# Performance work log

Measured on AMD Instinct MI355X. Metric: run time of the kernel, lower is better.

## Reference

```python
import jax, jax.numpy as jnp
import numpy as np

NA = 50000
NB = 50000
E = 800000
D = 256


def setup_inputs() -> dict:
    key = jax.random.key(0)
    ks = jax.random.split(key, 7)
    feature_a = jax.random.normal(ks[0], (NA, D), dtype=jnp.float32)
    feature_b = jax.random.normal(ks[1], (NB, D), dtype=jnp.float32)
    # Linear(b_dim, b_dim): store weight pre-transposed so new_emb = feature_b @ W + b
    W = jax.random.normal(ks[2], (D, D), dtype=jnp.float32) * (1.0 / np.sqrt(D))
    b = jnp.zeros((D,), dtype=jnp.float32)
    # kaiming-normal-ish init for attention vector a: [a_dim + b_dim, 1]
    a = jax.random.normal(ks[3], (2 * D, 1), dtype=jnp.float32) * np.sqrt(2.0 / (2 * D))
    edge_src = jnp.sort(jax.random.randint(ks[4], (E,), 0, NA, dtype=jnp.int32)).astype(jnp.int64)
    edge_dst = jax.random.randint(ks[5], (E,), 0, NB, dtype=jnp.int64)
    return {
        "feature_a": feature_a,
        "feature_b": feature_b,
        "W": W,
        "b": b,
        "a": a,
        "edge_src": edge_src,
        "edge_dst": edge_dst,
        "node_num_a": NA,
        "node_num_b": NB,
    }


def reference(feature_a, feature_b, W, b, a, edge_src, edge_dst, node_num_a, node_num_b):
    # new_emb = out_mlp_layer(feature_b)
    new_emb = feature_b @ W + b  # [Nb, D]

    # cat([feature_a[src], new_emb[dst]]) @ a  ==  (feature_a @ a_top)[src] + (new_emb @ a_bot)[dst]
    a_dim = feature_a.shape[1]
    a_top = a[:a_dim, 0]   # [a_dim]
    a_bot = a[a_dim:, 0]   # [b_dim]
    s_a = feature_a @ a_top   # [Na]
    s_b = new_emb @ a_bot     # [Nb]
    logits = s_a[edge_src] + s_b[edge_dst]  # [E]

    # exp(elu(x, alpha=0.1))
    elu = jnp.where(logits > 0, logits, 0.1 * jnp.expm1(logits))
    score = jnp.exp(elu)  # [E]

    # sparse mm: weighted aggregation of new_emb over edges, grouped by src
    msg = score[:, None] * new_emb[edge_dst]  # [E, D]
    agg = jax.ops.segment_sum(msg, edge_src, num_segments=node_num_a)       # [Na, D]
    row_sum = jax.ops.segment_sum(score, edge_src, num_segments=node_num_a)  # [Na]
    row_sum = jnp.where(row_sum == 0, 1.0, row_sum)[:, None]
    return agg / row_sum
```

## Files before the change

### kernel.cpp

```cpp
#include <hip/hip_runtime.h>
#include <cstdint>

#define NA_N 50000
#define NB_N 50000
#define NE_N 800000
#define DD 256
#define GEMM_NBLK 782
#define WT_NBLK   32
#define RS_NBLK   3125
#define SA_NBLK   3125

using bf8   = __attribute__((ext_vector_type(8))) short;
using f32x4 = __attribute__((ext_vector_type(4))) float;
using u16x8 = __attribute__((ext_vector_type(8))) ushort;

__device__ __forceinline__ ushort f2bf(float f) {
    uint u = __float_as_uint(f);
    uint r = (u + 0x7fffu + ((u >> 16) & 1u)) >> 16;
    return (ushort)r;
}
__device__ __forceinline__ float bf2f(ushort u) {
    return __uint_as_float(((uint)u) << 16);
}

__global__ __launch_bounds__(256) void prep_k(const float* __restrict__ W,
    ushort* __restrict__ Wt, const int* __restrict__ esrc,
    int* __restrict__ row_start, const float* __restrict__ fa,
    const float* __restrict__ a_top, float* __restrict__ s_a)
{
    const int t = threadIdx.x;
    if (blockIdx.x < WT_NBLK) {
        const int k0 = blockIdx.x * 8;
        u16x8 pack;
#pragma unroll
        for (int j = 0; j < 8; j++)
            pack[j] = f2bf(W[(size_t)(k0 + j) * DD + t]);
        *(u16x8*)(Wt + (size_t)t * DD + k0) = pack;
        return;
    }
    if (blockIdx.x < WT_NBLK + RS_NBLK) {
        int e = (blockIdx.x - WT_NBLK) * 256 + t;
        if (e >= NE_N) return;
        int s    = esrc[e];
        int prev = (e == 0) ? -1 : esrc[e - 1];
        for (int r = prev + 1; r <= s; r++) row_start[r] = e;
        if (e == NE_N - 1)
            for (int r = s + 1; r <= NA_N; r++) row_start[r] = NE_N;
        return;
    }
    const int row = (blockIdx.x - WT_NBLK - RS_NBLK) * 16 + (t >> 4);
    if (row >= NA_N) return;
    const f32x4* fr = (const f32x4*)(fa + (size_t)row * DD) + (t & 15) * 4;
    const f32x4* tv = (const f32x4*)a_top + (t & 15) * 4;
    float p = 0.f;
#pragma unroll
    for (int j = 0; j < 4; j++) {
        f32x4 x = fr[j], y = tv[j];
        p += x[0] * y[0] + x[1] * y[1] + x[2] * y[2] + x[3] * y[3];
    }
    p += __shfl_xor(p, 1, 64); p += __shfl_xor(p, 2, 64);
    p += __shfl_xor(p, 4, 64); p += __shfl_xor(p, 8, 64);
    if ((t & 15) == 0) s_a[row] = p;
}

__global__ __launch_bounds__(256) void gemm_mfma(
    const float* __restrict__ A, const ushort* __restrict__ Wt,
    const float* __restrict__ bias, const float* __restrict__ a_bot,
    ushort* __restrict__ C, float* __restrict__ s_b)
{
    __shared__ ushort As[64 * 264];
    __shared__ float  sdot[4][64];
    const int t  = threadIdx.x;
    const int r0 = blockIdx.x * 64;

#pragma unroll
    for (int i = 0; i < 16; i++) {
        int flat = i * 256 + t;
        int row  = flat >> 6;
        int c4   = flat & 63;
        int gr   = r0 + row; if (gr >= NB_N) gr = 0;
        float4 v = ((const float4*)(A + (size_t)gr * DD))[c4];
        ushort4 b;
        b.x = f2bf(v.x); b.y = f2bf(v.y); b.z = f2bf(v.z); b.w = f2bf(v.w);
        *(ushort4*)&As[row * 264 + c4 * 4] = b;
    }
    __syncthreads();

    const int lane = t & 63;
    const int wv   = t >> 6;
    const int lr   = lane & 15;
    const int lk   = (lane >> 4) * 8;
    const ushort* Wb = Wt + (size_t)(wv * 64 + lr) * DD + lk;

    f32x4 acc[4][4];
#pragma unroll
    for (int m = 0; m < 4; m++)
#pragma unroll
        for (int n = 0; n < 4; n++) acc[m][n] = (f32x4){0.f, 0.f, 0.f, 0.f};

    bf8 bbc[4], bbn[4];
#pragma unroll
    for (int n = 0; n < 4; n++)
        bbc[n] = *(const bf8*)(Wb + (size_t)n * 16 * DD);

#pragma unroll
    for (int ks = 0; ks < 8; ks++) {
        const int k0 = ks * 32;
        if (ks < 7) {
#pragma unroll
            for (int n = 0; n < 4; n++)
                bbn[n] = *(const bf8*)(Wb + (size_t)n * 16 * DD + k0 + 32);
        }
        bf8 af[4];
#pragma unroll
        for (int m = 0; m < 4; m++)
            af[m] = *(const bf8*)&As[(m * 16 + lr) * 264 + k0 + lk];
#pragma unroll
        for (int m = 0; m < 4; m++)
#pragma unroll
            for (int n = 0; n < 4; n++)
                acc[m][n] = __builtin_amdgcn_mfma_f32_16x16x32_bf16(
                    af[m], bbc[n], acc[m][n], 0, 0, 0);
#pragma unroll
        for (int n = 0; n < 4; n++) bbc[n] = bbn[n];
    }

    float abv[4];
#pragma unroll
    for (int n = 0; n < 4; n++) abv[n] = a_bot[wv * 64 + n * 16 + lr];

    float part[4][4];
#pragma unroll
    for (int m = 0; m < 4; m++)
#pragma unroll
        for (int r = 0; r < 4; r++) part[m][r] = 0.f;

#pragma unroll
    for (int m = 0; m < 4; m++)
#pragma unroll
        for (int n = 0; n < 4; n++) {
            int   col = wv * 64 + n * 16 + lr;
            float bv  = bias[col];
#pragma unroll
            for (int r = 0; r < 4; r++) {
                int   rowg = r0 + m * 16 + (lane >> 4) * 4 + r;
                float v    = acc[m][n][r] + bv;
                if (rowg < NB_N) C[(size_t)rowg * DD + col] = f2bf(v);
                part[m][r] = fmaf(v, abv[n], part[m][r]);
            }
        }

#pragma unroll
    for (int m = 0; m < 4; m++)
#pragma unroll
        for (int r = 0; r < 4; r++) {
#pragma unroll
            for (int off = 1; off < 16; off <<= 1)
                part[m][r] += __shfl_xor(part[m][r], off, 64);
        }
    if (lr == 0) {
#pragma unroll
        for (int m = 0; m < 4; m++)
#pragma unroll
            for (int r = 0; r < 4; r++)
                sdot[wv][m * 16 + (lane >> 4) * 4 + r] = part[m][r];
    }
    __syncthreads();
    if (t < 64) {
        int rowg = r0 + t;
        if (rowg < NB_N)
            s_b[rowg] = sdot[0][t] + sdot[1][t] + sdot[2][t] + sdot[3][t];
    }
}

__global__ __launch_bounds__(256) void edge_agg8(
    const int* __restrict__ edst, const int* __restrict__ row_start,
    const float* __restrict__ s_a, const float* __restrict__ sb,
    const ushort* __restrict__ emb, float* __restrict__ out)
{
    const int lane = threadIdx.x & 63;
    const int a    = blockIdx.x * 4 + (threadIdx.x >> 6);
    if (a >= NA_N) return;

    const float sa_a = s_a[a];
    const int g = lane >> 4;
    const int c = lane & 15;
    const int beg = row_start[a], end = row_start[a + 1];

    float accA[8], accB[8];
#pragma unroll
    for (int j = 0; j < 8; j++) { accA[j] = 0.f; accB[j] = 0.f; }
    float rs = 0.f;

    if (beg < end) {
        const int last = end - 1;

        int   pc  = beg + g;
        int   pn  = pc + 4;
        int   dc  = edst[min(pc, last)];
        int   dn  = edst[min(pn, last)];
        float sbc = sb[dc];
        float sbn = sb[dn];
        const ushort* rc = emb + (size_t)dc * DD + c * 16;
        u16x8 ua = *(const u16x8*)rc;
        u16x8 ub = *(const u16x8*)(rc + 8);

#pragma unroll 2
        for (int e = beg; e < end; e += 4) {
            const ushort* rn = emb + (size_t)dn * DD + c * 16;
            u16x8 na = *(const u16x8*)rn;
            u16x8 nb = *(const u16x8*)(rn + 8);
            int   p2  = pn + 4;
            int   d2  = edst[min(p2, last)];
            float sb2 = sb[d2];

            float lg = sa_a + sbc;
            float el = lg > 0.f ? lg : 0.1f * (__expf(lg) - 1.f);
            float s  = (pc < end) ? __expf(el) : 0.f;

#pragma unroll
            for (int j = 0; j < 8; j++) {
                accA[j] = fmaf(s, bf2f(ua[j]), accA[j]);
                accB[j] = fmaf(s, bf2f(ub[j]), accB[j]);
            }
            rs += s;

            pc = pn;  dc = dn;  sbc = sbn;
            ua = na;  ub = nb;
            pn = p2;  dn = d2;  sbn = sb2;
        }
    }

#pragma unroll
    for (int j = 0; j < 8; j++) {
        accA[j] += __shfl_xor(accA[j], 16, 64);
        accA[j] += __shfl_xor(accA[j], 32, 64);
        accB[j] += __shfl_xor(accB[j], 16, 64);
        accB[j] += __shfl_xor(accB[j], 32, 64);
    }
    rs += __shfl_xor(rs, 16, 64);
    rs += __shfl_xor(rs, 32, 64);

    if (g == 0) {
        const float inv = (rs == 0.f) ? 1.f : (1.f / rs);
        float* op = out + (size_t)a * DD + c * 16;
        float4 o0 = { accA[0] * inv, accA[1] * inv, accA[2] * inv, accA[3] * inv };
        float4 o1 = { accA[4] * inv, accA[5] * inv, accA[6] * inv, accA[7] * inv };
        float4 o2 = { accB[0] * inv, accB[1] * inv, accB[2] * inv, accB[3] * inv };
        float4 o3 = { accB[4] * inv, accB[5] * inv, accB[6] * inv, accB[7] * inv };
        *(float4*)(op + 0)  = o0;
        *(float4*)(op + 4)  = o1;
        *(float4*)(op + 8)  = o2;
        *(float4*)(op + 12) = o3;
    }
}

extern "C" void kernel_launch(void* const* d_in, const int* in_sizes, int n_in,
                              void* d_out, int out_size, void* d_ws, size_t ws_size,
                              hipStream_t stream)
{
    const float* fa   = (const float*)d_in[0];
    const float* fb   = (const float*)d_in[1];
    const float* W    = (const float*)d_in[2];
    const float* bias = (const float*)d_in[3];
    const float* avec = (const float*)d_in[4];
    const int*   esrc = (const int*)d_in[5];
    const int*   edst = (const int*)d_in[6];
    float*       out  = (float*)d_out;

    char*   ws        = (char*)d_ws;
    ushort* emb_b     = (ushort*)ws;
    float*  s_b       = (float*)(ws + (size_t)NB_N * DD * 2);
    int*    row_start = (int*)(s_b + NB_N);
    float*  s_a       = (float*)(row_start + NA_N + 2);
    ushort* Wt        = (ushort*)(s_a + NA_N);

    prep_k   <<<WT_NBLK + RS_NBLK + SA_NBLK, 256, 0, stream>>>(
        W, Wt, esrc, row_start, fa, avec, s_a);
    gemm_mfma<<<GEMM_NBLK, 256, 0, stream>>>(fb, Wt, bias, avec + DD,
                                             emb_b, s_b);
    edge_agg8<<<(NA_N + 3) / 4, 256, 0, stream>>>(edst, row_start, s_a,
                                                  s_b, emb_b, out);
}
```

Measured before the change: 105.3 us.

## Compute s_b from precomputed W·a_bot and swizzle GEMM shared-memory layout

Precomputes w2 = W·a_bot and c0 = bias·a_bot in an extra prep block. s_b is then taken as a dot product of each fp32 input row with w2, done during the GEMM's A-tile load, so the post-GEMM reduction, the shuffles and the second barrier go away. It also replaces the padded LDS layout with an XOR swizzle to avoid bank conflicts while using less shared memory. s_b now comes from fp32 inputs rather than the bf16-rounded GEMM output, which changes numerics slightly, and the single-block w2 computation adds a small serial piece to prep.

```diff
diff --git a/kernel.cpp b/kernel.cpp
--- a/kernel.cpp
+++ b/kernel.cpp
@@ -26,7 +26,9 @@
 __global__ __launch_bounds__(256) void prep_k(const float* __restrict__ W,
     ushort* __restrict__ Wt, const int* __restrict__ esrc,
     int* __restrict__ row_start, const float* __restrict__ fa,
-    const float* __restrict__ a_top, float* __restrict__ s_a)
+    const float* __restrict__ a_top, float* __restrict__ s_a,
+    const float* __restrict__ bias, const float* __restrict__ a_bot,
+    float* __restrict__ w2c0)
 {
     const int t = threadIdx.x;
     if (blockIdx.x < WT_NBLK) {
@@ -48,49 +50,75 @@
             for (int r = s + 1; r <= NA_N; r++) row_start[r] = NE_N;
         return;
     }
-    const int row = (blockIdx.x - WT_NBLK - RS_NBLK) * 16 + (t >> 4);
-    if (row >= NA_N) return;
-    const f32x4* fr = (const f32x4*)(fa + (size_t)row * DD) + (t & 15) * 4;
-    const f32x4* tv = (const f32x4*)a_top + (t & 15) * 4;
-    float p = 0.f;
-#pragma unroll
-    for (int j = 0; j < 4; j++) {
-        f32x4 x = fr[j], y = tv[j];
-        p += x[0] * y[0] + x[1] * y[1] + x[2] * y[2] + x[3] * y[3];
-    }
-    p += __shfl_xor(p, 1, 64); p += __shfl_xor(p, 2, 64);
-    p += __shfl_xor(p, 4, 64); p += __shfl_xor(p, 8, 64);
-    if ((t & 15) == 0) s_a[row] = p;
+    if (blockIdx.x < WT_NBLK + RS_NBLK + SA_NBLK) {
+        const int row = (blockIdx.x - WT_NBLK - RS_NBLK) * 16 + (t >> 4);
+        if (row >= NA_N) return;
+        const f32x4* fr = (const f32x4*)(fa + (size_t)row * DD) + (t & 15) * 4;
+        const f32x4* tv = (const f32x4*)a_top + (t & 15) * 4;
+        float p = 0.f;
+#pragma unroll
+        for (int j = 0; j < 4; j++) {
+            f32x4 x = fr[j], y = tv[j];
+            p += x[0] * y[0] + x[1] * y[1] + x[2] * y[2] + x[3] * y[3];
+        }
+        p += __shfl_xor(p, 1, 64); p += __shfl_xor(p, 2, 64);
+        p += __shfl_xor(p, 4, 64); p += __shfl_xor(p, 8, 64);
+        if ((t & 15) == 0) s_a[row] = p;
+        return;
+    }
+    {
+        const f32x4* wr = (const f32x4*)(W + (size_t)t * DD);
+        const f32x4* ab = (const f32x4*)a_bot;
+        float acc = 0.f;
+#pragma unroll 8
+        for (int j = 0; j < 64; j++) {
+            f32x4 x = wr[j], y = ab[j];
+            acc += x[0] * y[0] + x[1] * y[1] + x[2] * y[2] + x[3] * y[3];
+        }
+        w2c0[t] = acc;
+        if (t == 0) {
+            float c0 = 0.f;
+            for (int n = 0; n < DD; n++) c0 = fmaf(bias[n], a_bot[n], c0);
+            w2c0[DD] = c0;
+        }
+    }
 }
 
 __global__ __launch_bounds__(256) void gemm_mfma(
     const float* __restrict__ A, const ushort* __restrict__ Wt,
-    const float* __restrict__ bias, const float* __restrict__ a_bot,
+    const float* __restrict__ bias, const float* __restrict__ w2c0,
     ushort* __restrict__ C, float* __restrict__ s_b)
 {
-    __shared__ ushort As[64 * 264];
-    __shared__ float  sdot[4][64];
+    __shared__ ushort As[64 * 256];
     const int t  = threadIdx.x;
     const int r0 = blockIdx.x * 64;
+    const int wv = t >> 6;
+
+    const f32x4 w2v = ((const f32x4*)w2c0)[t & 63];
+    const float c0  = w2c0[DD];
 
 #pragma unroll
     for (int i = 0; i < 16; i++) {
-        int flat = i * 256 + t;
-        int row  = flat >> 6;
-        int c4   = flat & 63;
-        int gr   = r0 + row; if (gr >= NB_N) gr = 0;
+        int row = i * 4 + wv;
+        int c4  = t & 63;
+        int gr  = r0 + row; if (gr >= NB_N) gr = 0;
         float4 v = ((const float4*)(A + (size_t)gr * DD))[c4];
         ushort4 b;
         b.x = f2bf(v.x); b.y = f2bf(v.y); b.z = f2bf(v.z); b.w = f2bf(v.w);
-        *(ushort4*)&As[row * 264 + c4 * 4] = b;
+        uint o = (uint)(row * 512 + c4 * 8) ^ (uint)((row & 7) << 4);
+        *(ushort4*)((char*)As + o) = b;
+        float p = v.x * w2v[0] + v.y * w2v[1] + v.z * w2v[2] + v.w * w2v[3];
+        p += __shfl_xor(p, 1, 64);  p += __shfl_xor(p, 2, 64);
+        p += __shfl_xor(p, 4, 64);  p += __shfl_xor(p, 8, 64);
+        p += __shfl_xor(p, 16, 64); p += __shfl_xor(p, 32, 64);
+        if ((t & 63) == 0 && r0 + row < NB_N) s_b[r0 + row] = p + c0;
     }
     __syncthreads();
 
     const int lane = t & 63;
-    const int wv   = t >> 6;
     const int lr   = lane & 15;
-    const int lk   = (lane >> 4) * 8;
-    const ushort* Wb = Wt + (size_t)(wv * 64 + lr) * DD + lk;
+    const int lkb  = ((lane >> 4) << 4);
+    const ushort* Wb = Wt + (size_t)(wv * 64 + lr) * DD + (lane >> 4) * 8;
 
     f32x4 acc[4][4];
 #pragma unroll
@@ -105,16 +133,18 @@
 
 #pragma unroll
     for (int ks = 0; ks < 8; ks++) {
-        const int k0 = ks * 32;
         if (ks < 7) {
 #pragma unroll
             for (int n = 0; n < 4; n++)
-                bbn[n] = *(const bf8*)(Wb + (size_t)n * 16 * DD + k0 + 32);
+                bbn[n] = *(const bf8*)(Wb + (size_t)n * 16 * DD + ks * 32 + 32);
         }
         bf8 af[4];
 #pragma unroll
-        for (int m = 0; m < 4; m++)
-            af[m] = *(const bf8*)&As[(m * 16 + lr) * 264 + k0 + lk];
+        for (int m = 0; m < 4; m++) {
+            int  row = m * 16 + lr;
+            uint o   = (uint)(row * 512 + ks * 64 + lkb) ^ (uint)((row & 7) << 4);
+            af[m] = *(const bf8*)((const char*)As + o);
+        }
 #pragma unroll
         for (int m = 0; m < 4; m++)
 #pragma unroll
@@ -125,16 +155,6 @@
         for (int n = 0; n < 4; n++) bbc[n] = bbn[n];
     }
 
-    float abv[4];
-#pragma unroll
-    for (int n = 0; n < 4; n++) abv[n] = a_bot[wv * 64 + n * 16 + lr];
-
-    float part[4][4];
-#pragma unroll
-    for (int m = 0; m < 4; m++)
-#pragma unroll
-        for (int r = 0; r < 4; r++) part[m][r] = 0.f;
-
 #pragma unroll
     for (int m = 0; m < 4; m++)
 #pragma unroll
@@ -143,34 +163,11 @@
             float bv  = bias[col];
 #pragma unroll
             for (int r = 0; r < 4; r++) {
-                int   rowg = r0 + m * 16 + (lane >> 4) * 4 + r;
-                float v    = acc[m][n][r] + bv;
-                if (rowg < NB_N) C[(size_t)rowg * DD + col] = f2bf(v);
-                part[m][r] = fmaf(v, abv[n], part[m][r]);
+                int rowg = r0 + m * 16 + (lane >> 4) * 4 + r;
+                if (rowg < NB_N)
+                    C[(size_t)rowg * DD + col] = f2bf(acc[m][n][r] + bv);
             }
         }
-
-#pragma unroll
-    for (int m = 0; m < 4; m++)
-#pragma unroll
-        for (int r = 0; r < 4; r++) {
-#pragma unroll
-            for (int off = 1; off < 16; off <<= 1)
-                part[m][r] += __shfl_xor(part[m][r], off, 64);
-        }
-    if (lr == 0) {
-#pragma unroll
-        for (int m = 0; m < 4; m++)
-#pragma unroll
-            for (int r = 0; r < 4; r++)
-                sdot[wv][m * 16 + (lane >> 4) * 4 + r] = part[m][r];
-    }
-    __syncthreads();
-    if (t < 64) {
-        int rowg = r0 + t;
-        if (rowg < NB_N)
-            s_b[rowg] = sdot[0][t] + sdot[1][t] + sdot[2][t] + sdot[3][t];
-    }
 }
 
 __global__ __launch_bounds__(256) void edge_agg8(
@@ -273,12 +270,12 @@
     float*  s_b       = (float*)(ws + (size_t)NB_N * DD * 2);
     int*    row_start = (int*)(s_b + NB_N);
     float*  s_a       = (float*)(row_start + NA_N + 2);
-    ushort* Wt        = (ushort*)(s_a + NA_N);
-
-    prep_k   <<<WT_NBLK + RS_NBLK + SA_NBLK, 256, 0, stream>>>(
-        W, Wt, esrc, row_start, fa, avec, s_a);
-    gemm_mfma<<<GEMM_NBLK, 256, 0, stream>>>(fb, Wt, bias, avec + DD,
-                                             emb_b, s_b);
+    float*  w2c0      = s_a + NA_N;
+    ushort* Wt        = (ushort*)(w2c0 + DD + 2);
+
+    prep_k   <<<WT_NBLK + RS_NBLK + SA_NBLK + 1, 256, 0, stream>>>(
+        W, Wt, esrc, row_start, fa, avec, s_a, bias, avec + DD, w2c0);
+    gemm_mfma<<<GEMM_NBLK, 256, 0, stream>>>(fb, Wt, bias, w2c0, emb_b, s_b);
     edge_agg8<<<(NA_N + 3) / 4, 256, 0, stream>>>(edst, row_start, s_a,
                                                   s_b, emb_b, out);
 }
```

Result: slower. 126.1 us (+19.8%).
